# Optimization experiments

Measured on AMD Instinct MI355X. Metric: run time of the kernel, lower is better.

## Reference

```python
import jax, jax.numpy as jnp
import numpy as np

H = 128; B = 128; NA = 32; N = B * NA; NH = 4; DH = H // NH; F = 2 * H + 3


def _ln(x, g, b, eps=1e-5):
    m = x.mean(-1, keepdims=True)
    v = ((x - m) ** 2).mean(-1, keepdims=True)
    return (x - m) / jnp.sqrt(v + eps) * g + b


def _silu(x):
    return x * jax.nn.sigmoid(x)


def setup_inputs() -> dict:
    key = jax.random.key(0)
    ks = jax.random.split(key, 16)
    def rn(i, shape, s=0.05):
        return jax.random.normal(ks[i], shape, jnp.float32) * s
    return dict(
        num_atoms=jnp.full((B,), NA, dtype=jnp.int32),
        elems=jax.random.randint(ks[0], (N,), 0, 119),
        cell=jnp.tile(10.0 * jnp.eye(3, dtype=jnp.float32), (B, 1)),  # [3B,3]
        coord=jax.random.uniform(ks[1], (N, 3), jnp.float32, 1.0, 9.0),
        emb=rn(2, (119, H), 1.0),
        ln_in_g=jnp.ones((H,), jnp.float32), ln_in_b=jnp.zeros((H,), jnp.float32),
        attn_in_w=rn(3, (H, 3 * H)), attn_in_b=jnp.zeros((3 * H,), jnp.float32),
        attn_out_w=rn(4, (H, H)), attn_out_b=jnp.zeros((H,), jnp.float32),
        ce_w1=rn(5, (3, H)), ce_b1=jnp.zeros((H,), jnp.float32),
        ce_w2=rn(6, (H, H)), ce_b2=jnp.zeros((H,), jnp.float32),
        ln_feat_g=jnp.ones((F,), jnp.float32), ln_feat_b=jnp.zeros((F,), jnp.float32),
        op_w1=rn(7, (F, H)), op_b1=jnp.zeros((H,), jnp.float32),
        op_ln1_g=jnp.ones((H,), jnp.float32), op_ln1_b=jnp.zeros((H,), jnp.float32),
        res_w1=rn(8, (H, H)), res_b1=jnp.zeros((H,), jnp.float32),
        res_ln_g=jnp.ones((H,), jnp.float32), res_ln_b=jnp.zeros((H,), jnp.float32),
        res_w2=rn(9, (H, H)), res_b2=jnp.zeros((H,), jnp.float32),
        op_ln2_g=jnp.ones((H,), jnp.float32), op_ln2_b=jnp.zeros((H,), jnp.float32),
        op_w3=rn(10, (H, 3)), op_b3=jnp.zeros((3,), jnp.float32),
    )


def reference(num_atoms, elems, cell, coord, emb, ln_in_g, ln_in_b,
              attn_in_w, attn_in_b, attn_out_w, attn_out_b,
              ce_w1, ce_b1, ce_w2, ce_b2, ln_feat_g, ln_feat_b,
              op_w1, op_b1, op_ln1_g, op_ln1_b,
              res_w1, res_b1, res_ln_g, res_ln_b, res_w2, res_b2,
              op_ln2_g, op_ln2_b, op_w3, op_b3):
    n = coord.shape[0]
    # atom embedding + input LayerNorm
    x = _ln(emb[elems], ln_in_g, ln_in_b)
    # unbatched multihead self-attention over all atoms (seq_len = n)
    qkv = x @ attn_in_w + attn_in_b
    q, k, v = jnp.split(qkv, 3, axis=-1)
    q = q.reshape(n, NH, DH); k = k.reshape(n, NH, DH); v = v.reshape(n, NH, DH)
    a = jax.nn.softmax(jnp.einsum('qhd,khd->hqk', q, k) / np.float32(np.sqrt(DH)), axis=-1)
    x = jnp.einsum('hqk,khd->qhd', a, v).reshape(n, H) @ attn_out_w + attn_out_b
    # cell encoder on [3B,3] rows
    cf = _silu(cell @ ce_w1 + ce_b1) @ ce_w2 + ce_b2
    bidx = jnp.repeat(jnp.arange(num_atoms.shape[0]), num_atoms, total_repeat_length=n)
    # torch: cf.repeat(B,1)[batch_idx] == cf[batch_idx] since batch_idx < B
    comb = _ln(jnp.concatenate([x, cf[bidx], coord], axis=-1), ln_feat_g, ln_feat_b)
    # offset predictor
    h = _silu(_ln(comb @ op_w1 + op_b1, op_ln1_g, op_ln1_b))
    h = h + (_silu(_ln(h @ res_w1 + res_b1, res_ln_g, res_ln_b)) @ res_w2 + res_b2)
    h = _ln(h, op_ln2_g, op_ln2_b)
    offset = jnp.tanh(h @ op_w3 + op_b3) * 0.01
    perturbed = coord + offset
    # per-molecule clamp: segment gather of per-cell-row min/max replaces the python loop
    c3 = cell.reshape(-1, 3, 3)           # [B,3,3]
    cmin = c3.min(axis=2) + 1e-6          # [B,3]
    cmax = c3.max(axis=2) - 1e-6          # [B,3]
    return jnp.clip(perturbed, cmin[bidx], cmax[bidx])
```

## Files before the change

### kernel.cpp

```cpp
#include <hip/hip_runtime.h>
#include <hip/hip_bf16.h>
#include <math.h>
#include <stdint.h>

#define NATOMS 4096
#define HD     128
#define NHEAD  4
#define DHEAD  32
#define FDIM   259
#define BATCH  128
#define H3X    384
#define SPLIT  4

typedef __attribute__((ext_vector_type(8))) short short8;
typedef __attribute__((ext_vector_type(4))) float float4v;
typedef __attribute__((ext_vector_type(16))) float f32x16;

__device__ __forceinline__ ushort f2bf(float f) {
    uint32_t u = __float_as_uint(f);
    return (ushort)((u + 0x7fffu + ((u >> 16) & 1u)) >> 16);
}
__device__ __forceinline__ float b2f(ushort u) {
    return __uint_as_float(((uint32_t)u) << 16);
}
__device__ __forceinline__ f32x16 z16() {
    f32x16 v;
#pragma unroll
    for (int i = 0; i < 16; i++) v[i] = 0.f;
    return v;
}

__global__ __launch_bounds__(256) void k_setup(const float* __restrict__ qkvw,
                                               ushort* __restrict__ Wqkv) {
    int idx = blockIdx.x * 256 + threadIdx.x;
    int k = idx / 384, n = idx - k * 384;
    Wqkv[n * 128 + k] = f2bf(qkvw[idx]);
}

__global__ __launch_bounds__(256) void k_qkv(const int* __restrict__ elems,
                                             const float* __restrict__ emb,
                                             const float* __restrict__ lg,
                                             const float* __restrict__ lb,
                                             const ushort* __restrict__ Wt,
                                             const float* __restrict__ bias,
                                             ushort* __restrict__ Qb, ushort* __restrict__ Kb,
                                             ushort* __restrict__ VTb2) {
    __shared__ alignas(16) ushort Af[4][64][8];
    __shared__ alignas(16) ushort vt[128][16];
    const int t = threadIdx.x, w = t >> 6, lane = t & 63, quad = lane >> 4, lq = lane & 15;
    const int rg = blockIdx.x >> 1, half = blockIdx.x & 1;
    const int rb = rg * 16;
    {
        int row = t >> 4, seg = t & 15;
        int e = elems[rb + row];
        const float* ep = emb + (size_t)e * HD + seg * 8;
        float v[8]; float s = 0.f, ss = 0.f;
#pragma unroll
        for (int j = 0; j < 8; j++) { v[j] = ep[j]; s += v[j]; ss += v[j] * v[j]; }
#pragma unroll
        for (int m = 1; m < 16; m <<= 1) { s += __shfl_xor(s, m); ss += __shfl_xor(ss, m); }
        float mean = s * (1.f / HD);
        float inv = rsqrtf(ss * (1.f / HD) - mean * mean + 1e-5f);
        ushort o[8];
#pragma unroll
        for (int j = 0; j < 8; j++)
            o[j] = f2bf((v[j] - mean) * inv * lg[seg * 8 + j] + lb[seg * 8 + j]);
        *(uint4*)&Af[seg >> 2][(seg & 3) * 16 + row][0] = *(uint4*)o;
    }
    __syncthreads();
    float4v acc[3];
#pragma unroll
    for (int i = 0; i < 3; i++) acc[i] = (float4v){0.f, 0.f, 0.f, 0.f};
#pragma unroll
    for (int kt = 0; kt < 4; kt++) {
        short8 af = *(const short8*)&Af[kt][lane][0];
#pragma unroll
        for (int i = 0; i < 3; i++) {
            int nt = half * 12 + w * 3 + i;
            short8 wf = *(const short8*)(Wt + (size_t)(lq + 16 * nt) * HD + kt * 32 + quad * 8);
            acc[i] = __builtin_amdgcn_mfma_f32_16x16x32_bf16(af, wf, acc[i], 0, 0, 0);
        }
    }
#pragma unroll
    for (int i = 0; i < 3; i++) {
        int col = lq + 16 * (half * 12 + w * 3 + i);
        float bb = bias[col];
#pragma unroll
        for (int r = 0; r < 4; r++) {
            float c = acc[i][r] + bb;
            int rowin = quad * 4 + r;
            int row = rb + rowin;
            if (col < 128) {
                Qb[(size_t)(((col >> 5) * NATOMS) + row) * 32 + (col & 31)] = f2bf(c * 0.25503483f);
            } else if (col < 256) {
                int cc = col - 128;
                Kb[(size_t)(((cc >> 5) * NATOMS) + row) * 32 + (cc & 31)] = f2bf(c);
            } else {
                vt[col - 256][rowin] = f2bf(c);
            }
        }
    }
    __syncthreads();
    if (half == 1 && t < 128) {
        int hh = t >> 5, d = t & 31;
        uint4 a0 = *(const uint4*)&vt[t][0];
        uint4 a1 = *(const uint4*)&vt[t][8];
        ushort* dst = VTb2 + ((size_t)(hh * 64 + (rb >> 6)) * 32 + d) * 64 + (rb & 63);
        *(uint4*)(dst) = a0;
        *(uint4*)(dst + 8) = a1;
    }
}

__global__ __launch_bounds__(256) void k_attn(const ushort* __restrict__ Qb,
                                              const ushort* __restrict__ Kb,
                                              const ushort* __restrict__ VTb2,
                                              ushort* __restrict__ Opart,
                                              float* __restrict__ lpart,
                                              const int* __restrict__ num_atoms,
                                              const float* __restrict__ cell,
                                              const float* __restrict__ aow,
                                              const float* __restrict__ op1w,
                                              const float* __restrict__ r1w,
                                              const float* __restrict__ r2w,
                                              const float* __restrict__ ce_w1,
                                              const float* __restrict__ ce_b1,
                                              const float* __restrict__ ce_w2,
                                              const float* __restrict__ ce_b2,
                                              int* __restrict__ bidx,
                                              float* __restrict__ cmin,
                                              float* __restrict__ cmax,
                                              ushort* __restrict__ Wao,
                                              ushort* __restrict__ Wop1,
                                              ushort* __restrict__ Wr1,
                                              ushort* __restrict__ Wr2,
                                              float* __restrict__ CF) {
    __shared__ alignas(16) ushort P_s[4][32 * 72];
    __shared__ alignas(16) float OL[2][32 * 36];
    __shared__ float LL[2][32];
    const int t = threadIdx.x;

    if (blockIdx.z == SPLIT) {
        float* hs = (float*)&P_s[0][0];
        int* start = (int*)&P_s[1][0];
        const int mid = blockIdx.y * 64 + blockIdx.x;
        for (int j = mid * 256 + t; j < 86016; j += 65536) {
            if (j < 16384) {
                int k = j >> 7, n = j & 127;
                Wao[n * 128 + k] = f2bf(aow[j]);
            } else if (j < 49536) {
                int jj = j - 16384; int k = jj >> 7, n = jj & 127;
                Wop1[n * 288 + k] = f2bf(op1w[jj]);
            } else if (j < 53248) {
                int jj = j - 49536; int n = jj & 127, k = 259 + (jj >> 7);
                Wop1[n * 288 + k] = 0;
            } else if (j < 69632) {
                int jj = j - 53248; int k = jj >> 7, n = jj & 127;
                Wr1[n * 128 + k] = f2bf(r1w[jj]);
            } else {
                int jj = j - 69632; int k = jj >> 7, n = jj & 127;
                Wr2[n * 128 + k] = f2bf(r2w[jj]);
            }
        }
        if (mid < 128) {
            if (t < 128) {
                float c0 = cell[mid * 3 + 0], c1 = cell[mid * 3 + 1], c2 = cell[mid * 3 + 2];
                float h = c0 * ce_w1[t] + c1 * ce_w1[HD + t] + c2 * ce_w1[2 * HD + t] + ce_b1[t];
                h = h / (1.f + __expf(-h));
                hs[t] = h;
            }
            __syncthreads();
            if (t < 128) {
                float acc = ce_b2[t];
#pragma unroll 8
                for (int k = 0; k < HD; k++) acc += hs[k] * ce_w2[k * HD + t];
                CF[mid * HD + t] = acc;
            }
        } else if (mid == 128) {
            if (t == 0) {
                int pos = 0;
                for (int b = 0; b < BATCH; b++) { start[b] = pos; pos += num_atoms[b]; }
                start[BATCH] = pos;
            }
            __syncthreads();
            if (t < 128) {
                int s = min(start[t], NATOMS), e = min(start[t + 1], NATOMS);
                for (int j = s; j < e; j++) bidx[j] = t;
                if (t == 0) {
                    int total = min(start[BATCH], NATOMS);
                    for (int j = total; j < NATOMS; j++) bidx[j] = BATCH - 1;
                }
            }
            for (int rr = t; rr < BATCH * 3; rr += 256) {
                float a0 = cell[rr * 3 + 0], a1 = cell[rr * 3 + 1], a2 = cell[rr * 3 + 2];
                cmin[rr] = fminf(a0, fminf(a1, a2)) + 1e-6f;
                cmax[rr] = fmaxf(a0, fmaxf(a1, a2)) - 1e-6f;
            }
        }
        return;
    }

    const int w = t >> 6, lane = t & 63;
    const int l31 = lane & 31, hi = lane >> 5;
    const int qt = w & 1, kh2 = w >> 1;
    const int h = blockIdx.y, sp = blockIdx.z;
    const int q0 = blockIdx.x * 64;
    const int qrow = q0 + qt * 32 + l31;

    short8 qf0 = *(const short8*)(Qb + (size_t)(h * NATOMS + qrow) * 32 + hi * 8);
    short8 qf1 = *(const short8*)(Qb + (size_t)(h * NATOMS + qrow) * 32 + 16 + hi * 8);
    f32x16 O = z16();
    float lp = 0.f;
    ushort* Pw = &P_s[w][0];
    const int kstart = sp * (NATOMS / SPLIT) + kh2 * 64;

    for (int ck = 0; ck < (NATOMS / SPLIT) / 128; ck++) {
        int kb = kstart + ck * 128;
        const ushort* vbase = VTb2 + ((size_t)(h * 64 + (kb >> 6)) * 32 + l31) * 64;
#pragma unroll
        for (int kt = 0; kt < 2; kt++) {
            int kk = kb + kt * 32;
            const ushort* kp = Kb + (size_t)(h * NATOMS + kk + l31) * 32 + hi * 8;
            short8 kf0 = *(const short8*)(kp);
            short8 kf1 = *(const short8*)(kp + 16);
            f32x16 S = z16();
            S = __builtin_amdgcn_mfma_f32_32x32x16_bf16(kf0, qf0, S, 0, 0, 0);
            S = __builtin_amdgcn_mfma_f32_32x32x16_bf16(kf1, qf1, S, 0, 0, 0);
#pragma unroll
            for (int c = 0; c < 4; c++) {
                float p0 = exp2f(S[4 * c + 0]);
                float p1 = exp2f(S[4 * c + 1]);
                float p2 = exp2f(S[4 * c + 2]);
                float p3 = exp2f(S[4 * c + 3]);
                lp += (p0 + p1) + (p2 + p3);
                uint2 u;
                asm("v_cvt_pk_bf16_f32 %0, %1, %2" : "=v"(u.x) : "v"(p0), "v"(p1));
                asm("v_cvt_pk_bf16_f32 %0, %1, %2" : "=v"(u.y) : "v"(p2), "v"(p3));
                *(uint2*)(&Pw[l31 * 72 + kt * 32 + c * 8 + hi * 4]) = u;
            }
#pragma unroll
            for (int wd = 0; wd < 2; wd++) {
                int koff = kt * 32 + wd * 16;
                short8 vf = *(const short8*)(vbase + koff + hi * 8);
                short8 pf = *(const short8*)(&Pw[l31 * 72 + koff + hi * 8]);
                O = __builtin_amdgcn_mfma_f32_32x32x16_bf16(vf, pf, O, 0, 0, 0);
            }
        }
    }
    lp += __shfl_xor(lp, 32);
    if (kh2 == 0) {
#pragma unroll
        for (int c = 0; c < 4; c++) {
            float4 f = {O[4 * c + 0], O[4 * c + 1], O[4 * c + 2], O[4 * c + 3]};
            *(float4*)(&OL[qt][l31 * 36 + c * 8 + hi * 4]) = f;
        }
        if (hi == 0) LL[qt][l31] = lp;
    }
    __syncthreads();
    if (kh2 == 1) {
        lp += LL[qt][l31];
#pragma unroll
        for (int c = 0; c < 4; c++) {
            float4 f = *(const float4*)(&OL[qt][l31 * 36 + c * 8 + hi * 4]);
            float o0 = O[4 * c + 0] + f.x, o1 = O[4 * c + 1] + f.y;
            float o2 = O[4 * c + 2] + f.z, o3 = O[4 * c + 3] + f.w;
            uint2 u;
            u.x = (uint32_t)f2bf(o0) | ((uint32_t)f2bf(o1) << 16);
            u.y = (uint32_t)f2bf(o2) | ((uint32_t)f2bf(o3) << 16);
            *(uint2*)(Opart + (size_t)(sp * NATOMS + qrow) * HD + h * 32 + c * 8 + hi * 4) = u;
        }
        if (hi == 0) lpart[sp * (NHEAD * NATOMS) + h * NATOMS + qrow] = lp;
    }
}

__global__ __launch_bounds__(512) void k_back(
        const ushort* __restrict__ Opart, const float* __restrict__ lpart,
        const ushort* __restrict__ Wao, const float* __restrict__ aob,
        const float* __restrict__ CF, const float* __restrict__ coord,
        const int* __restrict__ bidx,
        const float* __restrict__ fg, const float* __restrict__ fb,
        const ushort* __restrict__ Wop1, const float* __restrict__ op1b,
        const float* __restrict__ l1g, const float* __restrict__ l1b,
        const ushort* __restrict__ Wr1, const float* __restrict__ r1b,
        const float* __restrict__ rlg, const float* __restrict__ rlb,
        const ushort* __restrict__ Wr2, const float* __restrict__ r2b,
        const float* __restrict__ l2g, const float* __restrict__ l2b,
        const float* __restrict__ w3, const float* __restrict__ b3,
        const float* __restrict__ cmin, const float* __restrict__ cmax,
        float* __restrict__ out) {
    __shared__ alignas(16) ushort AF1[9][64][8];
    __shared__ alignas(16) ushort AF2[4][64][8];
    __shared__ alignas(16) ushort AF3[4][64][8];
    __shared__ float RED[8][16][4];
    __shared__ float REDC[16][2];
    __shared__ float COORDS[16][3];
    const int t = threadIdx.x, w = t >> 6, lane = t & 63, quad = lane >> 4, lq = lane & 15;
    const int rb = blockIdx.x * 16;
    const int col = lq + 16 * w;

    const int arow = rb + lq;
    float4v a0 = {0.f, 0.f, 0.f, 0.f};
#pragma unroll
    for (int h = 0; h < 4; h++) {
        float l = 0.f;
#pragma unroll
        for (int s = 0; s < SPLIT; s++) l += lpart[s * (NHEAD * NATOMS) + h * NATOMS + arow];
        float inv = 1.f / l;
        float pv[8];
#pragma unroll
        for (int j = 0; j < 8; j++) pv[j] = 0.f;
#pragma unroll
        for (int s = 0; s < SPLIT; s++) {
            short8 ov = *(const short8*)(Opart + (size_t)(s * NATOMS + arow) * HD + h * 32 + quad * 8);
#pragma unroll
            for (int j = 0; j < 8; j++) pv[j] += b2f((ushort)ov[j]);
        }
        short8 af;
#pragma unroll
        for (int j = 0; j < 8; j++) af[j] = (short)f2bf(pv[j] * inv);
        short8 w0 = *(const short8*)(Wao + (size_t)col * HD + h * 32 + quad * 8);
        a0 = __builtin_amdgcn_mfma_f32_16x16x32_bf16(af, w0, a0, 0, 0, 0);
    }
    float x1[4];
#pragma unroll
    for (int r = 0; r < 4; r++) x1[r] = a0[r] + aob[col];

    float cfv[4];
#pragma unroll
    for (int r = 0; r < 4; r++) cfv[r] = CF[bidx[rb + quad * 4 + r] * HD + col];
#pragma unroll
    for (int r = 0; r < 4; r++) {
        float s1 = x1[r] + cfv[r];
        float s2 = x1[r] * x1[r] + cfv[r] * cfv[r];
#pragma unroll
        for (int m = 1; m < 16; m <<= 1) { s1 += __shfl_xor(s1, m); s2 += __shfl_xor(s2, m); }
        if (lq == 0) { RED[w][quad * 4 + r][0] = s1; RED[w][quad * 4 + r][1] = s2; }
    }
    if (t < 16) {
        float c0 = coord[(rb + t) * 3 + 0], c1 = coord[(rb + t) * 3 + 1], c2 = coord[(rb + t) * 3 + 2];
        COORDS[t][0] = c0; COORDS[t][1] = c1; COORDS[t][2] = c2;
        REDC[t][0] = c0 + c1 + c2; REDC[t][1] = c0 * c0 + c1 * c1 + c2 * c2;
    }
    if (t < 64) { uint4 z = {0, 0, 0, 0}; *(uint4*)&AF1[8][t][0] = z; }
    __syncthreads();
#pragma unroll
    for (int r = 0; r < 4; r++) {
        int ri = quad * 4 + r;
        float s1 = REDC[ri][0], s2 = REDC[ri][1];
#pragma unroll
        for (int ww = 0; ww < 8; ww++) { s1 += RED[ww][ri][0]; s2 += RED[ww][ri][1]; }
        float mn = s1 * (1.f / FDIM);
        float iv = rsqrtf(s2 * (1.f / FDIM) - mn * mn + 1e-5f);
        float vx = (x1[r] - mn) * iv * fg[col] + fb[col];
        float vc = (cfv[r] - mn) * iv * fg[col + 128] + fb[col + 128];
        AF1[col >> 5][((col >> 3) & 3) * 16 + ri][col & 7] = f2bf(vx);
        int c2 = col + 128;
        AF1[c2 >> 5][((c2 >> 3) & 3) * 16 + ri][c2 & 7] = f2bf(vc);
    }
    if (t < 16) {
        float s1 = REDC[t][0], s2 = REDC[t][1];
#pragma unroll
        for (int ww = 0; ww < 8; ww++) { s1 += RED[ww][t][0]; s2 += RED[ww][t][1]; }
        float mn = s1 * (1.f / FDIM);
        float iv = rsqrtf(s2 * (1.f / FDIM) - mn * mn + 1e-5f);
#pragma unroll
        for (int c = 0; c < 3; c++)
            AF1[8][t][c] = f2bf((COORDS[t][c] - mn) * iv * fg[256 + c] + fb[256 + c]);
    }
    __syncthreads();

    float4v cv = {0.f, 0.f, 0.f, 0.f};
#pragma unroll
    for (int kt = 0; kt < 9; kt++) {
        short8 af = *(const short8*)&AF1[kt][lane][0];
        short8 w0 = *(const short8*)(Wop1 + (size_t)col * 288 + kt * 32 + quad * 8);
        cv = __builtin_amdgcn_mfma_f32_16x16x32_bf16(af, w0, cv, 0, 0, 0);
    }
    float h0[4];
#pragma unroll
    for (int r = 0; r < 4; r++) {
        h0[r] = cv[r] + op1b[col];
        float s1 = h0[r], s2 = h0[r] * h0[r];
#pragma unroll
        for (int m = 1; m < 16; m <<= 1) { s1 += __shfl_xor(s1, m); s2 += __shfl_xor(s2, m); }
        if (lq == 0) { RED[w][quad * 4 + r][0] = s1; RED[w][quad * 4 + r][1] = s2; }
    }
    __syncthreads();
#pragma unroll
    for (int r = 0; r < 4; r++) {
        int ri = quad * 4 + r;
        float s1 = 0.f, s2 = 0.f;
#pragma unroll
        for (int ww = 0; ww < 8; ww++) { s1 += RED[ww][ri][0]; s2 += RED[ww][ri][1]; }
        float mn = s1 * (1.f / HD);
        float iv = rsqrtf(s2 * (1.f / HD) - mn * mn + 1e-5f);
        float o = (h0[r] - mn) * iv * l1g[col] + l1b[col];
        o = o / (1.f + __expf(-o));
        AF2[col >> 5][((col >> 3) & 3) * 16 + ri][col & 7] = f2bf(o);
    }
    __syncthreads();

    float4v dv = {0.f, 0.f, 0.f, 0.f};
#pragma unroll
    for (int kt = 0; kt < 4; kt++) {
        short8 af = *(const short8*)&AF2[kt][lane][0];
        short8 w0 = *(const short8*)(Wr1 + (size_t)col * HD + kt * 32 + quad * 8);
        dv = __builtin_amdgcn_mfma_f32_16x16x32_bf16(af, w0, dv, 0, 0, 0);
    }
    float e0[4];
#pragma unroll
    for (int r = 0; r < 4; r++) {
        e0[r] = dv[r] + r1b[col];
        float s1 = e0[r], s2 = e0[r] * e0[r];
#pragma unroll
        for (int m = 1; m < 16; m <<= 1) { s1 += __shfl_xor(s1, m); s2 += __shfl_xor(s2, m); }
        if (lq == 0) { RED[w][quad * 4 + r][0] = s1; RED[w][quad * 4 + r][1] = s2; }
    }
    __syncthreads();
#pragma unroll
    for (int r = 0; r < 4; r++) {
        int ri = quad * 4 + r;
        float s1 = 0.f, s2 = 0.f;
#pragma unroll
        for (int ww = 0; ww < 8; ww++) { s1 += RED[ww][ri][0]; s2 += RED[ww][ri][1]; }
        float mn = s1 * (1.f / HD);
        float iv = rsqrtf(s2 * (1.f / HD) - mn * mn + 1e-5f);
        float o = (e0[r] - mn) * iv * rlg[col] + rlb[col];
        o = o / (1.f + __expf(-o));
        AF3[col >> 5][((col >> 3) & 3) * 16 + ri][col & 7] = f2bf(o);
    }
    __syncthreads();

    float4v fv = {0.f, 0.f, 0.f, 0.f};
#pragma unroll
    for (int kt = 0; kt < 4; kt++) {
        short8 af = *(const short8*)&AF3[kt][lane][0];
        short8 w0 = *(const short8*)(Wr2 + (size_t)col * HD + kt * 32 + quad * 8);
        fv = __builtin_amdgcn_mfma_f32_16x16x32_bf16(af, w0, fv, 0, 0, 0);
    }
    float g0r[4];
#pragma unroll
    for (int r = 0; r < 4; r++) {
        int ri = quad * 4 + r;
        float rs = b2f(AF2[col >> 5][((col >> 3) & 3) * 16 + ri][col & 7]);
        g0r[r] = fv[r] + r2b[col] + rs;
        float s1 = g0r[r], s2 = g0r[r] * g0r[r];
#pragma unroll
        for (int m = 1; m < 16; m <<= 1) { s1 += __shfl_xor(s1, m); s2 += __shfl_xor(s2, m); }
        if (lq == 0) { RED[w][ri][0] = s1; RED[w][ri][1] = s2; }
    }
    __syncthreads();
    float tp[4][3];
#pragma unroll
    for (int r = 0; r < 4; r++) {
        int ri = quad * 4 + r;
        float s1 = 0.f, s2 = 0.f;
#pragma unroll
        for (int ww = 0; ww < 8; ww++) { s1 += RED[ww][ri][0]; s2 += RED[ww][ri][1]; }
        float mn = s1 * (1.f / HD);
        float iv = rsqrtf(s2 * (1.f / HD) - mn * mn + 1e-5f);
        float h2 = (g0r[r] - mn) * iv * l2g[col] + l2b[col];
#pragma unroll
        for (int c = 0; c < 3; c++) {
            float v = h2 * w3[col * 3 + c];
#pragma unroll
            for (int m = 1; m < 16; m <<= 1) v += __shfl_xor(v, m);
            tp[r][c] = v;
        }
    }
    __syncthreads();
    if (lq == 0) {
#pragma unroll
        for (int r = 0; r < 4; r++) {
            RED[w][quad * 4 + r][0] = tp[r][0];
            RED[w][quad * 4 + r][1] = tp[r][1];
            RED[w][quad * 4 + r][2] = tp[r][2];
        }
    }
    __syncthreads();
    if (t < 16) {
        int bi = bidx[rb + t];
#pragma unroll
        for (int c = 0; c < 3; c++) {
            float sv = 0.f;
#pragma unroll
            for (int ww = 0; ww < 8; ww++) sv += RED[ww][t][c];
            float off = tanhf(sv + b3[c]) * 0.01f;
            float pert = COORDS[t][c] + off;
            pert = fminf(fmaxf(pert, cmin[bi * 3 + c]), cmax[bi * 3 + c]);
            out[(rb + t) * 3 + c] = pert;
        }
    }
}

extern "C" void kernel_launch(void* const* d_in, const int* in_sizes, int n_in,
                              void* d_out, int out_size, void* d_ws, size_t ws_size,
                              hipStream_t stream) {
    const int* num_atoms = (const int*)d_in[0];
    const int* elems = (const int*)d_in[1];
    const float* cell = (const float*)d_in[2];
    const float* coord = (const float*)d_in[3];
    const float* emb = (const float*)d_in[4];
    const float* ln_in_g = (const float*)d_in[5];
    const float* ln_in_b = (const float*)d_in[6];
    const float* attn_in_w = (const float*)d_in[7];
    const float* attn_in_b = (const float*)d_in[8];
    const float* attn_out_w = (const float*)d_in[9];
    const float* attn_out_b = (const float*)d_in[10];
    const float* ce_w1 = (const float*)d_in[11];
    const float* ce_b1 = (const float*)d_in[12];
    const float* ce_w2 = (const float*)d_in[13];
    const float* ce_b2 = (const float*)d_in[14];
    const float* ln_feat_g = (const float*)d_in[15];
    const float* ln_feat_b = (const float*)d_in[16];
    const float* op_w1 = (const float*)d_in[17];
    const float* op_b1 = (const float*)d_in[18];
    const float* op_ln1_g = (const float*)d_in[19];
    const float* op_ln1_b = (const float*)d_in[20];
    const float* res_w1 = (const float*)d_in[21];
    const float* res_b1 = (const float*)d_in[22];
    const float* res_ln_g = (const float*)d_in[23];
    const float* res_ln_b = (const float*)d_in[24];
    const float* res_w2 = (const float*)d_in[25];
    const float* res_b2 = (const float*)d_in[26];
    const float* op_ln2_g = (const float*)d_in[27];
    const float* op_ln2_b = (const float*)d_in[28];
    const float* op_w3 = (const float*)d_in[29];
    const float* op_b3 = (const float*)d_in[30];

    char* ws = (char*)d_ws;
    const size_t MB = 1u << 20;
    ushort* Qb = (ushort*)(ws);
    ushort* Kb = (ushort*)(ws + 1 * MB);
    ushort* VTb2 = (ushort*)(ws + 2 * MB);
    ushort* Opart = (ushort*)(ws + 3 * MB);
    float* lpart = (float*)(ws + 7 * MB);
    int* bidx = (int*)(ws + 7 * MB + (256u << 10));
    float* cmin = (float*)(ws + 7 * MB + (272u << 10));
    float* cmax = (float*)(ws + 7 * MB + (274u << 10));
    float* CF = (float*)(ws + 7 * MB + (276u << 10));
    ushort* Wqkv = (ushort*)(ws + 7 * MB + (340u << 10));
    ushort* Wao = (ushort*)(ws + 7 * MB + (436u << 10));
    ushort* Wop1 = (ushort*)(ws + 7 * MB + (468u << 10));
    ushort* Wr1 = (ushort*)(ws + 7 * MB + (540u << 10));
    ushort* Wr2 = (ushort*)(ws + 7 * MB + (572u << 10));

    k_setup<<<192, 256, 0, stream>>>(attn_in_w, Wqkv);
    k_qkv<<<512, 256, 0, stream>>>(elems, emb, ln_in_g, ln_in_b, Wqkv, attn_in_b,
                                   Qb, Kb, VTb2);
    k_attn<<<dim3(NATOMS / 64, NHEAD, SPLIT + 1), 256, 0, stream>>>(
        Qb, Kb, VTb2, Opart, lpart,
        num_atoms, cell, attn_out_w, op_w1, res_w1, res_w2,
        ce_w1, ce_b1, ce_w2, ce_b2, bidx, cmin, cmax,
        Wao, Wop1, Wr1, Wr2, CF);
    k_back<<<256, 512, 0, stream>>>(Opart, lpart, Wao, attn_out_b, CF, coord, bidx,
                                    ln_feat_g, ln_feat_b, Wop1, op_b1, op_ln1_g, op_ln1_b,
                                    Wr1, res_b1, res_ln_g, res_ln_b, Wr2, res_b2,
                                    op_ln2_g, op_ln2_b, op_w3, op_b3, cmin, cmax,
                                    (float*)d_out);
}
```

Measured before the change: 175.4 us.

## Fuse QKV weight conversion into k_qkv and raise MFMA wave priority

Removes the separate k_setup launch that transposed and converted the QKV weights to bf16. Each k_qkv block now converts its half of the fp32 weights into a swizzled LDS tile in MFMA fragment order, which saves a kernel launch and a global round trip. The cost is that every one of the 512 blocks re-reads 96K fp32 weights with strided loads, and the block uses about 48KB more LDS. Separately, s_setprio is wrapped around the MFMAs in the attention loop so waves issuing matrix ops get scheduling priority over waves doing exp work.

```diff
diff --git a/kernel.cpp b/kernel.cpp
--- a/kernel.cpp
+++ b/kernel.cpp
@@ -30,26 +30,35 @@
     return v;
 }
 
-__global__ __launch_bounds__(256) void k_setup(const float* __restrict__ qkvw,
-                                               ushort* __restrict__ Wqkv) {
-    int idx = blockIdx.x * 256 + threadIdx.x;
-    int k = idx / 384, n = idx - k * 384;
-    Wqkv[n * 128 + k] = f2bf(qkvw[idx]);
-}
-
 __global__ __launch_bounds__(256) void k_qkv(const int* __restrict__ elems,
                                              const float* __restrict__ emb,
                                              const float* __restrict__ lg,
                                              const float* __restrict__ lb,
-                                             const ushort* __restrict__ Wt,
+                                             const float* __restrict__ qkvw,
                                              const float* __restrict__ bias,
                                              ushort* __restrict__ Qb, ushort* __restrict__ Kb,
                                              ushort* __restrict__ VTb2) {
+    __shared__ alignas(16) ushort Wl[48 * 512];
     __shared__ alignas(16) ushort Af[4][64][8];
     __shared__ alignas(16) ushort vt[128][16];
     const int t = threadIdx.x, w = t >> 6, lane = t & 63, quad = lane >> 4, lq = lane & 15;
     const int rg = blockIdx.x >> 1, half = blockIdx.x & 1;
     const int rb = rg * 16;
+
+#pragma unroll
+    for (int m = 0; m < 12; m++) {
+        int s = t + 256 * m;
+        int chunk = s >> 6, l = s & 63;
+        int ntl = chunk >> 2, kt = chunk & 3;
+        int q8 = (l >> 4) * 8, lqq = l & 15;
+        int n = half * 192 + ntl * 16 + lqq;
+        int k0 = kt * 32 + q8;
+        ushort o[8];
+#pragma unroll
+        for (int j = 0; j < 8; j++) o[j] = f2bf(qkvw[(k0 + j) * H3X + n]);
+        *(uint4*)&Wl[(chunk << 9) + (l << 3)] = *(uint4*)o;
+    }
+
     {
         int row = t >> 4, seg = t & 15;
         int e = elems[rb + row];
@@ -68,6 +77,7 @@
         *(uint4*)&Af[seg >> 2][(seg & 3) * 16 + row][0] = *(uint4*)o;
     }
     __syncthreads();
+
     float4v acc[3];
 #pragma unroll
     for (int i = 0; i < 3; i++) acc[i] = (float4v){0.f, 0.f, 0.f, 0.f};
@@ -76,8 +86,7 @@
         short8 af = *(const short8*)&Af[kt][lane][0];
 #pragma unroll
         for (int i = 0; i < 3; i++) {
-            int nt = half * 12 + w * 3 + i;
-            short8 wf = *(const short8*)(Wt + (size_t)(lq + 16 * nt) * HD + kt * 32 + quad * 8);
+            short8 wf = *(const short8*)&Wl[((((w * 3 + i) << 2) + kt) << 9) + (lane << 3)];
             acc[i] = __builtin_amdgcn_mfma_f32_16x16x32_bf16(af, wf, acc[i], 0, 0, 0);
         }
     }
@@ -223,8 +232,10 @@
             short8 kf0 = *(const short8*)(kp);
             short8 kf1 = *(const short8*)(kp + 16);
             f32x16 S = z16();
+            __builtin_amdgcn_s_setprio(1);
             S = __builtin_amdgcn_mfma_f32_32x32x16_bf16(kf0, qf0, S, 0, 0, 0);
             S = __builtin_amdgcn_mfma_f32_32x32x16_bf16(kf1, qf1, S, 0, 0, 0);
+            __builtin_amdgcn_s_setprio(0);
 #pragma unroll
             for (int c = 0; c < 4; c++) {
                 float p0 = exp2f(S[4 * c + 0]);
@@ -242,7 +253,9 @@
                 int koff = kt * 32 + wd * 16;
                 short8 vf = *(const short8*)(vbase + koff + hi * 8);
                 short8 pf = *(const short8*)(&Pw[l31 * 72 + koff + hi * 8]);
+                __builtin_amdgcn_s_setprio(1);
                 O = __builtin_amdgcn_mfma_f32_32x32x16_bf16(vf, pf, O, 0, 0, 0);
+                __builtin_amdgcn_s_setprio(0);
             }
         }
     }
@@ -538,14 +551,12 @@
     float* cmin = (float*)(ws + 7 * MB + (272u << 10));
     float* cmax = (float*)(ws + 7 * MB + (274u << 10));
     float* CF = (float*)(ws + 7 * MB + (276u << 10));
-    ushort* Wqkv = (ushort*)(ws + 7 * MB + (340u << 10));
     ushort* Wao = (ushort*)(ws + 7 * MB + (436u << 10));
     ushort* Wop1 = (ushort*)(ws + 7 * MB + (468u << 10));
     ushort* Wr1 = (ushort*)(ws + 7 * MB + (540u << 10));
     ushort* Wr2 = (ushort*)(ws + 7 * MB + (572u << 10));
 
-    k_setup<<<192, 256, 0, stream>>>(attn_in_w, Wqkv);
-    k_qkv<<<512, 256, 0, stream>>>(elems, emb, ln_in_g, ln_in_b, Wqkv, attn_in_b,
+    k_qkv<<<512, 256, 0, stream>>>(elems, emb, ln_in_g, ln_in_b, attn_in_w, attn_in_b,
                                    Qb, Kb, VTb2);
     k_attn<<<dim3(NATOMS / 64, NHEAD, SPLIT + 1), 256, 0, stream>>>(
         Qb, Kb, VTb2, Opart, lpart,
```

Result: no change. 172.1 us, median of 2 (-1.8%).
